# Optimization experiments

Hardware: AMD Instinct MI355X
Metric: run time of the kernel (lower is better)

The kernel has to match this reference:

```python
import jax, jax.numpy as jnp
import numpy as np

INO, INN, HID = 128, 128, 64

def _xavier(key, shape):
    fan_in, fan_out = shape[0], shape[1]
    limit = float(np.sqrt(6.0 / (fan_in + fan_out)))
    return jax.random.uniform(key, shape, jnp.float32, -limit, limit)

def setup_inputs() -> dict:
    key = jax.random.key(0)
    k1, k2, k3, k4 = jax.random.split(key, 4)
    xo = jax.random.normal(k1, (512, INO), jnp.float32)
    xn = jax.random.normal(k2, (2048, INN), jnp.float32)
    W1 = _xavier(k3, (INO + INN, HID))  # Linear(ino+inn, hidden).weight.T
    b1 = jnp.zeros((HID,), jnp.float32)
    W2 = _xavier(k4, (HID, 1))          # Linear(hidden, 1).weight.T
    b2 = jnp.zeros((1,), jnp.float32)
    return {"xo": xo, "xn": xn, "W1": W1, "b1": b1, "W2": W2, "b2": b2}

def reference(xo, xn, W1, b1, W2, b2):
    # cat([xo_expanded, xn_expanded]) @ W1 == xo @ W1[:ino] + xn @ W1[ino:]
    ino = xo.shape[1]
    pre = xo @ W1[:ino]                      # [B, H]
    pre_n = xn @ W1[ino:]                    # [N, H]
    h = jax.nn.leaky_relu(pre[:, None, :] + pre_n[None, :, :] + b1, 0.2)  # [B, N, H]
    scores = jnp.einsum('bnh,h->bn', h, W2[:, 0]) + b2[0]                  # [B, N]
    att = jax.nn.softmax(scores, axis=1)                                   # [B, N]
    return att @ xn                                                        # [B, inn]
```

## Files before the change

### kernel.cpp

```cpp
#include <hip/hip_runtime.h>
#include <math.h>

#define INO 128
#define INN 128
#define HID 64
#define NB  512
#define NN  2048
#define TB  4
#define NCH 8
#define NPC (NN / NCH)

__global__ __launch_bounds__(256) void pre_kernel(
    const float* __restrict__ xo, const float* __restrict__ xn,
    const float* __restrict__ W1, const float* __restrict__ b1,
    float* __restrict__ pre)
{
    int t = blockIdx.x * blockDim.x + threadIdx.x;
    int row = t >> 6;
    int h = t & 63;
    if (row >= NB + NN) return;
    const float* x;
    const float* w;
    float a0, a1 = 0.f, a2 = 0.f, a3 = 0.f;
    if (row < NB) { x = xo + row * INO;        w = W1;             a0 = b1[h]; }
    else          { x = xn + (row - NB) * INN; w = W1 + INO * HID; a0 = 0.f;  }
    const float4* x4 = (const float4*)x;
#pragma unroll
    for (int k4 = 0; k4 < INO / 4; ++k4) {
        float4 xv = x4[k4];
        int kb = k4 * 4;
        a0 = fmaf(xv.x, w[(kb + 0) * HID + h], a0);
        a1 = fmaf(xv.y, w[(kb + 1) * HID + h], a1);
        a2 = fmaf(xv.z, w[(kb + 2) * HID + h], a2);
        a3 = fmaf(xv.w, w[(kb + 3) * HID + h], a3);
    }
    pre[row * HID + h] = (a0 + a1) + (a2 + a3);
}

__global__ __launch_bounds__(256) void score_pv_kernel(
    const float* __restrict__ pre, const float* __restrict__ xn,
    const float* __restrict__ W2,
    float* __restrict__ smax, float* __restrict__ ssum,
    float* __restrict__ part)
{
    const int bt = blockIdx.x >> 3;
    const int ch = blockIdx.x & 7;
    const int b0 = bt * TB;
    const int n0 = ch * NPC;
    const int tid = threadIdx.x;
    const int lane = tid & 63, wid = tid >> 6;

    __shared__ float  s_po[TB][HID];
    __shared__ float  s_w2[HID];
    __shared__ float4 s_p4[NPC];
    __shared__ float  s_red[4][2 * TB];
    __shared__ float  s_part[2][TB][INN];

    const float* pre_n = pre + NB * HID;
    s_po[tid >> 6][tid & 63] = pre[(b0 + (tid >> 6)) * HID + (tid & 63)];
    if (tid < HID) s_w2[tid] = W2[tid];
    __syncthreads();

    float acc[TB] = {0.f, 0.f, 0.f, 0.f};
    const float4* pn = (const float4*)(pre_n + (n0 + tid) * HID);
#pragma unroll 4
    for (int j = 0; j < HID / 4; ++j) {
        float4 v = pn[j];
#pragma unroll
        for (int hh = 0; hh < 4; ++hh) {
            float w = s_w2[4 * j + hh];
            float e = (&v.x)[hh];
#pragma unroll
            for (int b = 0; b < TB; ++b) {
                float t = s_po[b][4 * j + hh] + e;
                acc[b] = fmaf(fmaxf(t, 0.2f * t), w, acc[b]);
            }
        }
    }

    float m[TB];
#pragma unroll
    for (int b = 0; b < TB; ++b) {
        float v = acc[b];
#pragma unroll
        for (int o = 32; o > 0; o >>= 1) v = fmaxf(v, __shfl_xor(v, o, 64));
        if (lane == 0) s_red[wid][b] = v;
    }
    __syncthreads();
#pragma unroll
    for (int b = 0; b < TB; ++b)
        m[b] = fmaxf(fmaxf(s_red[0][b], s_red[1][b]),
                     fmaxf(s_red[2][b], s_red[3][b]));

    float p[TB];
#pragma unroll
    for (int b = 0; b < TB; ++b) {
        p[b] = __expf(acc[b] - m[b]);
        float s = p[b];
#pragma unroll
        for (int o = 32; o > 0; o >>= 1) s += __shfl_xor(s, o, 64);
        if (lane == 0) s_red[wid][TB + b] = s;
    }
    s_p4[tid] = make_float4(p[0], p[1], p[2], p[3]);
    __syncthreads();
    if (tid < TB) {
        float sm = s_red[0][TB + tid] + s_red[1][TB + tid] +
                   s_red[2][TB + tid] + s_red[3][TB + tid];
        smax[ch * NB + b0 + tid] = m[tid];
        ssum[ch * NB + b0 + tid] = sm;
    }

    const int c = tid & 127;
    const int g = tid >> 7;
    float facc[TB] = {0.f, 0.f, 0.f, 0.f};
    const float* xp = xn + (n0 + g * (NPC / 2)) * INN + c;
#pragma unroll 8
    for (int k = 0; k < NPC / 2; ++k) {
        float xv = xp[k * INN];
        float4 pv = s_p4[g * (NPC / 2) + k];
        facc[0] = fmaf(pv.x, xv, facc[0]);
        facc[1] = fmaf(pv.y, xv, facc[1]);
        facc[2] = fmaf(pv.z, xv, facc[2]);
        facc[3] = fmaf(pv.w, xv, facc[3]);
    }
#pragma unroll
    for (int b = 0; b < TB; ++b) s_part[g][b][c] = facc[b];
    __syncthreads();
    {
        int idx = tid * 2;
        int b = idx >> 7, cc = idx & 127;
        float2 o;
        o.x = s_part[0][b][cc]     + s_part[1][b][cc];
        o.y = s_part[0][b][cc + 1] + s_part[1][b][cc + 1];
        *(float2*)&part[(ch * NB + b0 + b) * INN + cc] = o;
    }
}

__global__ __launch_bounds__(256) void combine_kernel(
    const float* __restrict__ smax, const float* __restrict__ ssum,
    const float* __restrict__ part, float* __restrict__ out)
{
    int idx = blockIdx.x * 256 + threadIdx.x;
    int b = idx >> 7, c = idx & 127;
    float mv[NCH];
    float M = -1e30f;
#pragma unroll
    for (int ch = 0; ch < NCH; ++ch) {
        mv[ch] = smax[ch * NB + b];
        M = fmaxf(M, mv[ch]);
    }
    float den = 0.f, num = 0.f;
#pragma unroll
    for (int ch = 0; ch < NCH; ++ch) {
        float sc = __expf(mv[ch] - M);
        den = fmaf(ssum[ch * NB + b], sc, den);
        num = fmaf(part[(ch * NB + b) * INN + c], sc, num);
    }
    out[idx] = num / den;
}

extern "C" void kernel_launch(void* const* d_in, const int* in_sizes, int n_in,
                              void* d_out, int out_size, void* d_ws, size_t ws_size,
                              hipStream_t stream) {
    const float* xo = (const float*)d_in[0];
    const float* xn = (const float*)d_in[1];
    const float* W1 = (const float*)d_in[2];
    const float* b1 = (const float*)d_in[3];
    const float* W2 = (const float*)d_in[4];
    float* out = (float*)d_out;

    float* pre  = (float*)d_ws;
    float* smax = pre + (NB + NN) * HID;
    float* ssum = smax + NCH * NB;
    float* part = ssum + NCH * NB;

    const int total = (NB + NN) * HID;
    pre_kernel<<<(total + 255) / 256, 256, 0, stream>>>(xo, xn, W1, b1, pre);
    score_pv_kernel<<<(NB / TB) * NCH, 256, 0, stream>>>(pre, xn, W2, smax, ssum, part);
    combine_kernel<<<(NB * INN) / 256, 256, 0, stream>>>(smax, ssum, part, out);
}
```

Before: 93.80 us.

## Vectorize PV accumulation with float4 columns and read pre/W2 directly

Each thread in the P·V stage now loads a float4 of xn and accumulates a 4x4 register tile, using 8 row groups instead of 2. The partial sums are then reduced across those groups through shared memory. The score loop drops its shared-memory staging of the query pre-activations and W2 and reads them straight from global memory as uniform loads, which removes one barrier. The aim is fewer load instructions and more reuse per load, at the cost of more registers and a larger reduction step.

```diff
diff --git a/kernel.cpp b/kernel.cpp
--- a/kernel.cpp
+++ b/kernel.cpp
@@ -50,16 +50,12 @@
     const int tid = threadIdx.x;
     const int lane = tid & 63, wid = tid >> 6;
 
-    __shared__ float  s_po[TB][HID];
-    __shared__ float  s_w2[HID];
     __shared__ float4 s_p4[NPC];
     __shared__ float  s_red[4][2 * TB];
-    __shared__ float  s_part[2][TB][INN];
+    __shared__ float4 s_part4[8][TB][INN / 4];
 
     const float* pre_n = pre + NB * HID;
-    s_po[tid >> 6][tid & 63] = pre[(b0 + (tid >> 6)) * HID + (tid & 63)];
-    if (tid < HID) s_w2[tid] = W2[tid];
-    __syncthreads();
+    const float* po = pre + b0 * HID;
 
     float acc[TB] = {0.f, 0.f, 0.f, 0.f};
     const float4* pn = (const float4*)(pre_n + (n0 + tid) * HID);
@@ -68,11 +64,12 @@
         float4 v = pn[j];
 #pragma unroll
         for (int hh = 0; hh < 4; ++hh) {
-            float w = s_w2[4 * j + hh];
-            float e = (&v.x)[hh];
+            const int h = 4 * j + hh;
+            const float w = W2[h];
+            const float e = (&v.x)[hh];
 #pragma unroll
             for (int b = 0; b < TB; ++b) {
-                float t = s_po[b][4 * j + hh] + e;
+                float t = po[b * HID + h] + e;
                 acc[b] = fmaf(fmaxf(t, 0.2f * t), w, acc[b]);
             }
         }
@@ -110,29 +107,45 @@
         ssum[ch * NB + b0 + tid] = sm;
     }
 
-    const int c = tid & 127;
-    const int g = tid >> 7;
-    float facc[TB] = {0.f, 0.f, 0.f, 0.f};
-    const float* xp = xn + (n0 + g * (NPC / 2)) * INN + c;
+    const int c4 = tid & 31;
+    const int g  = tid >> 5;
+    float4 f[TB];
+#pragma unroll
+    for (int b = 0; b < TB; ++b) f[b] = make_float4(0.f, 0.f, 0.f, 0.f);
+    const float* xp = xn + (size_t)(n0 + g * 32) * INN + c4 * 4;
 #pragma unroll 8
-    for (int k = 0; k < NPC / 2; ++k) {
-        float xv = xp[k * INN];
-        float4 pv = s_p4[g * (NPC / 2) + k];
-        facc[0] = fmaf(pv.x, xv, facc[0]);
-        facc[1] = fmaf(pv.y, xv, facc[1]);
-        facc[2] = fmaf(pv.z, xv, facc[2]);
-        facc[3] = fmaf(pv.w, xv, facc[3]);
+    for (int k = 0; k < 32; ++k) {
+        float4 xv = *(const float4*)(xp + (size_t)k * INN);
+        float4 pv = s_p4[g * 32 + k];
+        f[0].x = fmaf(pv.x, xv.x, f[0].x);
+        f[0].y = fmaf(pv.x, xv.y, f[0].y);
+        f[0].z = fmaf(pv.x, xv.z, f[0].z);
+        f[0].w = fmaf(pv.x, xv.w, f[0].w);
+        f[1].x = fmaf(pv.y, xv.x, f[1].x);
+        f[1].y = fmaf(pv.y, xv.y, f[1].y);
+        f[1].z = fmaf(pv.y, xv.z, f[1].z);
+        f[1].w = fmaf(pv.y, xv.w, f[1].w);
+        f[2].x = fmaf(pv.z, xv.x, f[2].x);
+        f[2].y = fmaf(pv.z, xv.y, f[2].y);
+        f[2].z = fmaf(pv.z, xv.z, f[2].z);
+        f[2].w = fmaf(pv.z, xv.w, f[2].w);
+        f[3].x = fmaf(pv.w, xv.x, f[3].x);
+        f[3].y = fmaf(pv.w, xv.y, f[3].y);
+        f[3].z = fmaf(pv.w, xv.z, f[3].z);
+        f[3].w = fmaf(pv.w, xv.w, f[3].w);
     }
 #pragma unroll
-    for (int b = 0; b < TB; ++b) s_part[g][b][c] = facc[b];
+    for (int b = 0; b < TB; ++b) s_part4[g][b][c4] = f[b];
     __syncthreads();
-    {
-        int idx = tid * 2;
-        int b = idx >> 7, cc = idx & 127;
-        float2 o;
-        o.x = s_part[0][b][cc]     + s_part[1][b][cc];
-        o.y = s_part[0][b][cc + 1] + s_part[1][b][cc + 1];
-        *(float2*)&part[(ch * NB + b0 + b) * INN + cc] = o;
+    if (tid < TB * (INN / 4)) {
+        int b = tid >> 5, cc = tid & 31;
+        float4 s = make_float4(0.f, 0.f, 0.f, 0.f);
+#pragma unroll
+        for (int gg = 0; gg < 8; ++gg) {
+            float4 v = s_part4[gg][b][cc];
+            s.x += v.x; s.y += v.y; s.z += v.z; s.w += v.w;
+        }
+        *(float4*)&part[(size_t)(ch * NB + b0 + b) * INN + cc * 4] = s;
     }
 }
 
@@ -154,7 +167,7 @@
     for (int ch = 0; ch < NCH; ++ch) {
         float sc = __expf(mv[ch] - M);
         den = fmaf(ssum[ch * NB + b], sc, den);
-        num = fmaf(part[(ch * NB + b) * INN + c], sc, num);
+        num = fmaf(part[(size_t)(ch * NB + b) * INN + c], sc, num);
     }
     out[idx] = num / den;
 }
```

Measured after the change: 87.61 us. -6.6%, faster.
